# Kernel tuning notes

Measured on AMD Instinct MI355X. Metric: run time of the kernel, lower is better.

Reference implementation:

```python
import jax, jax.numpy as jnp
import numpy as np
from jax import lax

# Dims: B=batch, Cin=in_channel, Ch=channel (bottleneck), Br=breadth (num expert kernels)
B, Cin, Ch, Br, H, W = 16, 256, 128, 8, 64, 64


def setup_inputs() -> dict:
    key = jax.random.key(0)
    ks = jax.random.split(key, 6)
    sc = lambda k, shape: jax.random.normal(k, shape, jnp.float32) * 0.05
    return {
        "x": jax.random.normal(ks[0], (B, Cin, H, W), jnp.float32),
        # SwitchedConv #1: 3x3, in_channel -> channel, breadth expert kernels
        "W1": sc(ks[1], (Br, Ch, Cin, 3, 3)),
        "b1": jnp.zeros((Ch,), jnp.float32),
        # lambda coupler #1: 1x1 projection in_channel -> breadth (per-pixel routing)
        "Wc1": sc(ks[2], (Br, Cin)),
        "bc1": jnp.zeros((Br,), jnp.float32),
        # SwitchedConv #2: 1x1, channel -> in_channel
        "W2": sc(ks[3], (Br, Cin, Ch, 1, 1)),
        "b2": jnp.zeros((Cin,), jnp.float32),
        # lambda coupler #2: 1x1 projection channel -> breadth
        "Wc2": sc(ks[4], (Br, Ch)),
        "bc2": jnp.zeros((Br,), jnp.float32),
    }


def _switched_conv(x, Wk, b, Wc, bc, pad):
    """Input-conditioned mixture of `breadth` conv kernels.

    The coupler (1x1 projection of x to breadth logits, softmax over breadth)
    produces per-pixel mixture weights; each expert kernel's conv output is
    combined per-pixel with these weights.
    x: [B, Cin, H, W]; Wk: [Br, Cout, Cin, k, k]
    """
    br, cout, cin, k, _ = Wk.shape
    bsz, _, h, w = x.shape
    # per-pixel routing weights over the breadth dim: [B, Br, H, W]
    sel = jax.nn.softmax(jnp.einsum('bihw,gi->bghw', x, Wc) + bc[None, :, None, None], axis=1)
    # all breadth branches in one grouped-output conv: [B, Br*Cout, H, W]
    y = lax.conv_general_dilated(
        x, Wk.reshape(br * cout, cin, k, k),
        window_strides=(1, 1), padding=[(pad, pad), (pad, pad)],
        dimension_numbers=('NCHW', 'OIHW', 'NCHW'))
    y = y.reshape(bsz, br, cout, h, w)
    # selection-weighted reduction over breadth + bias
    return jnp.einsum('bgchw,bghw->bchw', y, sel) + b[None, :, None, None]


def reference(x, W1, b1, Wc1, bc1, W2, b2, Wc2, bc2):
    h = jax.nn.relu(x)
    h = _switched_conv(h, W1, b1, Wc1, bc1, pad=1)  # 3x3 switched conv
    h = jax.nn.relu(h)
    h = _switched_conv(h, W2, b2, Wc2, bc2, pad=0)  # 1x1 switched conv
    return h + x  # residual add
```

## Files before the change

kernel.cpp:

```cpp
#include <hip/hip_runtime.h>
#include <hip/hip_bf16.h>
#include <cstdint>

typedef _Float16 h8 __attribute__((ext_vector_type(8)));
typedef _Float16 h4 __attribute__((ext_vector_type(4)));
typedef float    f4 __attribute__((ext_vector_type(4)));
typedef float    fx16 __attribute__((ext_vector_type(16)));


#define GLD16(src, dst) __builtin_amdgcn_global_load_lds( \
    (const __attribute__((address_space(1))) void*)(src), \
    (__attribute__((address_space(3))) void*)(dst), 16, 0, 0)

__global__ __launch_bounds__(256) void prep_w_k(const float* __restrict__ W1,
        const float* __restrict__ W2, _Float16* __restrict__ W1r,
        _Float16* __restrict__ W2r) {
    int o8 = blockIdx.x * 256 + threadIdx.x;
    if (o8 < 294912) {
        int sq = o8 & 3;
        int c  = (o8 >> 2) & 127;
        int g  = (o8 >> 9) & 7;
        int tk = o8 >> 12;
        int tap = tk % 9, cik = tk / 9;
        int s = sq ^ ((c >> 1) & 3);
        int ci0 = cik * 32 + s * 8;
        const float* src = W1 + ((size_t)(g * 128 + c) * 256 + ci0) * 9 + tap;
        h8 v;
        #pragma unroll
        for (int e = 0; e < 8; ++e) v[e] = (_Float16)src[e * 9];
        *(h8*)(W1r + (size_t)o8 * 8) = v;
    } else {
        int ow = o8 - 294912;
        int sg = ow & 3;
        int co = (ow >> 2) & 255;
        int kc = (ow >> 10) & 3;
        int g  = ow >> 12;
        const float* src = W2 + ((size_t)(g * 256 + co) * 128) + kc * 32 + sg * 8;
        h8 v;
        #pragma unroll
        for (int e = 0; e < 8; ++e) v[e] = (_Float16)src[e];
        *(h8*)(W2r + (size_t)ow * 8) = v;
    }
}

__global__ __launch_bounds__(256) void prep_x_k(const float* __restrict__ x,
        const float* __restrict__ Wc1, const float* __restrict__ bc1,
        float* __restrict__ sel1) {
    __shared__ float wc[2048];
    int t = threadIdx.x;
    for (int i = t; i < 2048; i += 256) wc[i] = Wc1[i];
    __syncthreads();
    int pix = blockIdx.x * 256 + t;
    int b = pix >> 12, p = pix & 4095;
    const float* xp = x + (size_t)b * 1048576 + p;
    float lg[8] = {0.f,0.f,0.f,0.f,0.f,0.f,0.f,0.f};
    for (int c = 0; c < 256; ++c) {
        float v = fmaxf(xp[(size_t)c * 4096], 0.f);
        #pragma unroll
        for (int g = 0; g < 8; ++g) lg[g] += wc[g * 256 + c] * v;
    }
    float m = -1e30f;
    #pragma unroll
    for (int g = 0; g < 8; ++g) { lg[g] += bc1[g]; m = fmaxf(m, lg[g]); }
    float sum = 0.f;
    #pragma unroll
    for (int g = 0; g < 8; ++g) { lg[g] = __expf(lg[g] - m); sum += lg[g]; }
    float inv = 1.f / sum;
    #pragma unroll
    for (int g = 0; g < 8; ++g)
        sel1[(size_t)(b * 8 + g) * 4096 + p] = lg[g] * inv;
}

__global__ __launch_bounds__(512, 2) void conv1_k(const float* __restrict__ x,
        const _Float16* __restrict__ W1r, const float* __restrict__ sel1,
        const float* __restrict__ b1, _Float16* __restrict__ hr) {
    __shared__ _Float16 wt[2][32768];
    __shared__ _Float16 xs[12296];
    int t = threadIdx.x;
    int b = blockIdx.y, yt = blockIdx.x;
    int y0 = yt * 4;
    int w = t >> 6, l = t & 63;
    int wm = w >> 2, wn = w & 3;
    int l31 = l & 31, kq2 = l >> 5;
    if (t < 8) xs[12288 + t] = (_Float16)0.f;

    fx16 acc[2][2];
    #pragma unroll
    for (int m = 0; m < 2; ++m)
        #pragma unroll
        for (int n = 0; n < 2; ++n)
            #pragma unroll
            for (int e = 0; e < 16; ++e) acc[m][n][e] = 0.f;

    {
        const _Float16* srcw = W1r + (size_t)t * 8;
        _Float16* dw = wt[0] + t * 8;
        #pragma unroll
        for (int it = 0; it < 8; ++it)
            GLD16(srcw + it * 4096, dw + it * 4096);
    }

    int px[2];
    #pragma unroll
    for (int nf = 0; nf < 2; ++nf) px[nf] = wn * 64 + nf * 32 + l31;
    bool e0 = (l31 == 0), e63 = (l31 == 31);
    int afo[2][2];
    #pragma unroll
    for (int m = 0; m < 2; ++m)
        #pragma unroll
        for (int kc = 0; kc < 2; ++kc) {
            int c = wm * 64 + m * 32 + l31;
            afo[m][kc] = c * 32 + (((kc * 2 + kq2) ^ ((c >> 1) & 3)) * 8);
        }
    int ba[2][3][2];
    #pragma unroll
    for (int nf = 0; nf < 2; ++nf)
        #pragma unroll
        for (int kx = 0; kx < 3; ++kx) {
            int rz = px[nf] + kx - 1;
            #pragma unroll
            for (int kc = 0; kc < 2; ++kc)
                ba[nf][kx][kc] = rz * 32 + (((kc * 2 + kq2) ^ ((rz >> 1) & 3)) * 8);
        }
    h8 selv[2];
    #pragma unroll
    for (int nf = 0; nf < 2; ++nf)
        #pragma unroll
        for (int g = 0; g < 8; ++g)
            selv[nf][g] = (_Float16)sel1[(size_t)(b * 8 + g) * 4096 + yt * 256 + px[nf]];

    #pragma unroll 1
    for (int ci = 0; ci < 8; ++ci) {
        __syncthreads();
        if (t < 384) {
            int r = t >> 6, col = t & 63;
            int rc = r * 64 + col;
            int yi = y0 - 1 + r;
            _Float16* dx = xs + rc * 32;
            int rx = (rc >> 1) & 3;
            if (yi >= 0 && yi < 64) {
                const float* xp = x + ((size_t)(b * 256 + ci * 32)) * 4096 + yi * 64 + col;
                float v[32];
                #pragma unroll
                for (int c2 = 0; c2 < 32; ++c2)
                    v[c2] = fmaxf(xp[(size_t)c2 * 4096], 0.f);
                #pragma unroll
                for (int qq = 0; qq < 4; ++qq) {
                    h8 hv;
                    #pragma unroll
                    for (int e = 0; e < 8; ++e) hv[e] = (_Float16)v[qq * 8 + e];
                    *(h8*)(dx + (qq ^ rx) * 8) = hv;
                }
            } else {
                const h8 HZ = {};
                #pragma unroll
                for (int qq = 0; qq < 4; ++qq)
                    *(h8*)(dx + (qq ^ rx) * 8) = HZ;
            }
        }
        #pragma unroll 1
        for (int ky = 0; ky < 3; ++ky) {
            #pragma unroll
            for (int kx = 0; kx < 3; ++kx) {
                int grp = ci * 9 + ky * 3 + kx;
                __syncthreads();
                if (grp < 71) {
                    const _Float16* srcw = W1r + (size_t)(grp + 1) * 32768 + t * 8;
                    _Float16* dw = wt[(grp + 1) & 1] + t * 8;
                    #pragma unroll
                    for (int it = 0; it < 8; ++it)
                        GLD16(srcw + it * 4096, dw + it * 4096);
                }
                h8 bfr[2][2];
                #pragma unroll
                for (int nf = 0; nf < 2; ++nf)
                    #pragma unroll
                    for (int kc = 0; kc < 2; ++kc) {
                        int a = ba[nf][kx][kc] + ky * 2048;
                        if (kx == 0 && nf == 0) a = e0 ? 12288 : a;
                        if (kx == 2 && nf == 1) a = e63 ? 12288 : a;
                        bfr[nf][kc] = *(const h8*)(xs + a);
                    }
                const _Float16* wp = wt[grp & 1];
                #pragma unroll
                for (int g = 0; g < 8; ++g) {
                    h8 a00 = *(const h8*)(wp + g * 4096 + afo[0][0]);
                    h8 a01 = *(const h8*)(wp + g * 4096 + afo[0][1]);
                    h8 a10 = *(const h8*)(wp + g * 4096 + afo[1][0]);
                    h8 a11 = *(const h8*)(wp + g * 4096 + afo[1][1]);
                    #pragma unroll
                    for (int nf = 0; nf < 2; ++nf) {
                        _Float16 sg = selv[nf][g];
                        h8 b0 = bfr[nf][0] * sg;
                        h8 b1v = bfr[nf][1] * sg;
                        acc[0][nf] = __builtin_amdgcn_mfma_f32_32x32x16_f16(
                            a00, b0, acc[0][nf], 0, 0, 0);
                        acc[1][nf] = __builtin_amdgcn_mfma_f32_32x32x16_f16(
                            a10, b0, acc[1][nf], 0, 0, 0);
                        acc[0][nf] = __builtin_amdgcn_mfma_f32_32x32x16_f16(
                            a01, b1v, acc[0][nf], 0, 0, 0);
                        acc[1][nf] = __builtin_amdgcn_mfma_f32_32x32x16_f16(
                            a11, b1v, acc[1][nf], 0, 0, 0);
                    }
                }
            }
        }
    }
    #pragma unroll
    for (int m = 0; m < 2; ++m)
        #pragma unroll
        for (int nf = 0; nf < 2; ++nf) {
            size_t pg = ((size_t)(b * 4096 + yt * 256 + px[nf])) * 128;
            #pragma unroll
            for (int q = 0; q < 4; ++q) {
                int c0 = wm * 64 + m * 32 + q * 8 + kq2 * 4;
                f4 bb = *(const f4*)(b1 + c0);
                h4 hv;
                #pragma unroll
                for (int r = 0; r < 4; ++r)
                    hv[r] = (_Float16)fmaxf(acc[m][nf][q * 4 + r] + bb[r], 0.f);
                *(h4*)(hr + pg + c0) = hv;
            }
        }
}

__global__ __launch_bounds__(256, 2) void conv2_k(const _Float16* __restrict__ hr,
        const _Float16* __restrict__ W2r, const float* __restrict__ Wc2,
        const float* __restrict__ bc2, const float* __restrict__ b2,
        const float* __restrict__ x, float* __restrict__ out) {
    __shared__ _Float16 hs[64 * 128];
    __shared__ _Float16 wt[2][256 * 32];
    __shared__ float wc[1024];
    __shared__ float red[2048];
    __shared__ float selw[512];
    int t = threadIdx.x;
    int bid = blockIdx.x;
    int b = bid >> 6, p0 = (bid & 63) * 64;
    int l = t & 63, w = t >> 6;
    int wm = w >> 1, wn = w & 1;
    int l15 = l & 15, sl = l >> 4;
    int swl = (l15 & 7) << 3;
    const f4 FZ = {0.f, 0.f, 0.f, 0.f};
    f4 acce[8][2], accf[8][2];
    #pragma unroll
    for (int m = 0; m < 8; ++m)
        #pragma unroll
        for (int n = 0; n < 2; ++n) { acce[m][n] = FZ; accf[m][n] = FZ; }
    for (int i = t; i < 1024; i += 256) wc[i] = Wc2[i];
    {
        int px = t >> 2, qq = t & 3;
        const _Float16* src = hr + (size_t)(b * 4096 + p0 + px) * 128 + qq * 32;
        #pragma unroll
        for (int u = 0; u < 4; ++u)
            *(h8*)(hs + ((px * 128 + qq * 32 + u * 8) ^ ((px & 7) << 3)))
                = *(const h8*)(src + u * 8);
    }
    h8 wr[4];
    auto load_w = [&](int T) {
        const _Float16* srcw = W2r + (size_t)T * 8192;
        #pragma unroll
        for (int it = 0; it < 4; ++it)
            wr[it] = *(const h8*)(srcw + (size_t)(it * 256 + t) * 8);
    };
    auto write_w = [&](int bf) {
        #pragma unroll
        for (int it = 0; it < 4; ++it) {
            int cc = it * 256 + t;
            int c = cc >> 2, q = cc & 3;
            *(h8*)(wt[bf] + ((c * 32 + q * 8) ^ ((c & 7) << 3))) = wr[it];
        }
    };
    load_w(0);
    __syncthreads();
    {
        int px = t >> 2, qq = t & 3;
        float lg[8] = {0.f,0.f,0.f,0.f,0.f,0.f,0.f,0.f};
        #pragma unroll
        for (int u = 0; u < 4; ++u) {
            h8 v = *(const h8*)(hs + ((px * 128 + qq * 32 + u * 8) ^ ((px & 7) << 3)));
            #pragma unroll
            for (int e = 0; e < 8; ++e) {
                float f = (float)v[e];
                int c = qq * 32 + u * 8 + e;
                #pragma unroll
                for (int g = 0; g < 8; ++g) lg[g] += wc[g * 128 + c] * f;
            }
        }
        #pragma unroll
        for (int g = 0; g < 8; ++g) red[(px * 8 + g) * 4 + qq] = lg[g];
    }
    __syncthreads();
    if (t < 64) {
        float lg[8]; float m = -1e30f;
        #pragma unroll
        for (int g = 0; g < 8; ++g) {
            lg[g] = red[(t*8+g)*4+0] + red[(t*8+g)*4+1]
                  + red[(t*8+g)*4+2] + red[(t*8+g)*4+3] + bc2[g];
            m = fmaxf(m, lg[g]);
        }
        float sum = 0.f;
        #pragma unroll
        for (int g = 0; g < 8; ++g) { lg[g] = __expf(lg[g] - m); sum += lg[g]; }
        float inv = 1.f / sum;
        #pragma unroll
        for (int g = 0; g < 8; ++g) selw[t * 8 + g] = lg[g] * inv;
    }
    write_w(0);
    __syncthreads();
    float selr[8][2];
    #pragma unroll
    for (int g = 0; g < 8; ++g)
        #pragma unroll
        for (int n = 0; n < 2; ++n)
            selr[g][n] = selw[(wn * 32 + n * 16 + l15) * 8 + g];
    int afo[8];
    #pragma unroll
    for (int m = 0; m < 8; ++m) {
        int c = wm * 128 + m * 16 + l15;
        afo[m] = ((c * 32 + sl * 8) ^ swl);
    }
    int buf = 0;
    #pragma unroll 1
    for (int T = 0; T < 32; ++T) {
        bool hn = (T < 31);
        if (hn) load_w(T + 1);
        __syncthreads();
        int kc = (T & 3) * 32;
        h8 bfv[2];
        #pragma unroll
        for (int n = 0; n < 2; ++n) {
            int px = wn * 32 + n * 16 + l15;
            bfv[n] = *(const h8*)(hs + ((px * 128 + kc + sl * 8) ^ ((px & 7) << 3)));
        }
        #pragma unroll
        for (int m = 0; m < 8; ++m) {
            h8 af = *(const h8*)(wt[buf] + afo[m]);
            #pragma unroll
            for (int n = 0; n < 2; ++n)
                acce[m][n] = __builtin_amdgcn_mfma_f32_16x16x32_f16(
                    af, bfv[n], acce[m][n], 0, 0, 0);
        }
        if ((T & 3) == 3) {
            int g = T >> 2;
            #pragma unroll
            for (int n = 0; n < 2; ++n)
                #pragma unroll
                for (int m = 0; m < 8; ++m) {
                    accf[m][n] += selr[g][n] * acce[m][n];
                    acce[m][n] = FZ;
                }
        }
        if (hn) write_w(buf ^ 1);
        buf ^= 1;
    }
    #pragma unroll
    for (int m = 0; m < 8; ++m) {
        int c0 = wm * 128 + m * 16 + sl * 4;
        f4 bb = *(const f4*)(b2 + c0);
        #pragma unroll
        for (int n = 0; n < 2; ++n) {
            int px = wn * 32 + n * 16 + l15;
            size_t o = (size_t)(b * 256 + c0) * 4096 + p0 + px;
            #pragma unroll
            for (int r = 0; r < 4; ++r)
                out[o + (size_t)r * 4096] = accf[m][n][r] + bb[r] + x[o + (size_t)r * 4096];
        }
    }
}

extern "C" void kernel_launch(void* const* d_in, const int* in_sizes, int n_in,
                              void* d_out, int out_size, void* d_ws, size_t ws_size,
                              hipStream_t stream) {
    const float* x   = (const float*)d_in[0];
    const float* W1  = (const float*)d_in[1];
    const float* b1  = (const float*)d_in[2];
    const float* Wc1 = (const float*)d_in[3];
    const float* bc1 = (const float*)d_in[4];
    const float* W2  = (const float*)d_in[5];
    const float* b2  = (const float*)d_in[6];
    const float* Wc2 = (const float*)d_in[7];
    const float* bc2 = (const float*)d_in[8];
    float* out = (float*)d_out;
    char* ws = (char*)d_ws;
    _Float16* hr  = (_Float16*)(ws);
    _Float16* W1r = (_Float16*)(ws + 16777216);
    _Float16* W2r = (_Float16*)(ws + 21495808);
    float* sel1   = (float*)(ws + 22020096);

    hipLaunchKernelGGL(prep_w_k, dim3(1280), dim3(256), 0, stream, W1, W2, W1r, W2r);
    hipLaunchKernelGGL(prep_x_k, dim3(256), dim3(256), 0, stream, x, Wc1, bc1, sel1);
    hipLaunchKernelGGL(conv1_k, dim3(16, 16), dim3(512), 0, stream, x, W1r, sel1, b1, hr);
    hipLaunchKernelGGL(conv2_k, dim3(1024), dim3(256), 0, stream, hr, W2r, Wc2, bc2, b2, x, out);
}
```

Before: 348.0 us.

## Pipeline conv1 weight staging in finer chunks with register prefetch

Splits each tap's weight tile into four 2-group chunks and rotates them through a three-buffer LDS ring, issuing async global-to-LDS loads two chunks ahead. A-fragments for the next chunk are preloaded into registers (FA/FB ping-pong) while MFMAs run on the current ones. LDS use drops from 64K to 24K halfs. The cost is four barriers per tap instead of one, plus more register pressure from the 16 preloaded fragments.

```diff
diff --git a/kernel.cpp b/kernel.cpp
--- a/kernel.cpp
+++ b/kernel.cpp
@@ -71,10 +71,38 @@
         sel1[(size_t)(b * 8 + g) * 4096 + p] = lg[g] * inv;
 }
 
+#define MFMA_BLOCK(F, GP) do { \
+    _Pragma("unroll") \
+    for (int gl_ = 0; gl_ < 2; ++gl_) { \
+        _Pragma("unroll") \
+        for (int kc_ = 0; kc_ < 2; ++kc_) { \
+            _Pragma("unroll") \
+            for (int nf_ = 0; nf_ < 2; ++nf_) { \
+                h8 bs_ = bfr[nf_][kc_] * selv[nf_][(GP) * 2 + gl_]; \
+                acc[0][nf_] = __builtin_amdgcn_mfma_f32_32x32x16_f16( \
+                    F[gl_ * 4 + kc_ * 2 + 0], bs_, acc[0][nf_], 0, 0, 0); \
+                acc[1][nf_] = __builtin_amdgcn_mfma_f32_32x32x16_f16( \
+                    F[gl_ * 4 + kc_ * 2 + 1], bs_, acc[1][nf_], 0, 0, 0); \
+            } } } \
+} while (0)
+
+#define PRELOAD(BI, F) do { \
+    const _Float16* wp_ = wt[BI]; \
+    _Pragma("unroll") \
+    for (int gl_ = 0; gl_ < 2; ++gl_) { \
+        _Pragma("unroll") \
+        for (int kc_ = 0; kc_ < 2; ++kc_) { \
+            _Pragma("unroll") \
+            for (int m_ = 0; m_ < 2; ++m_) \
+                F[gl_ * 4 + kc_ * 2 + m_] = \
+                    *(const h8*)(wp_ + gl_ * 4096 + afo[m_][kc_]); \
+        } } \
+} while (0)
+
 __global__ __launch_bounds__(512, 2) void conv1_k(const float* __restrict__ x,
         const _Float16* __restrict__ W1r, const float* __restrict__ sel1,
         const float* __restrict__ b1, _Float16* __restrict__ hr) {
-    __shared__ _Float16 wt[2][32768];
+    __shared__ _Float16 wt[3][8192];
     __shared__ _Float16 xs[12296];
     int t = threadIdx.x;
     int b = blockIdx.y, yt = blockIdx.x;
@@ -92,13 +120,12 @@
             #pragma unroll
             for (int e = 0; e < 16; ++e) acc[m][n][e] = 0.f;
 
-    {
-        const _Float16* srcw = W1r + (size_t)t * 8;
-        _Float16* dw = wt[0] + t * 8;
-        #pragma unroll
-        for (int it = 0; it < 8; ++it)
-            GLD16(srcw + it * 4096, dw + it * 4096);
-    }
+    auto stage_w = [&](int P, int bi) {
+        const _Float16* srcw = W1r + (size_t)P * 8192 + t * 8;
+        _Float16* dw = wt[bi] + t * 8;
+        GLD16(srcw, dw);
+        GLD16(srcw + 4096, dw + 4096);
+    };
 
     int px[2];
     #pragma unroll
@@ -129,9 +156,16 @@
         for (int g = 0; g < 8; ++g)
             selv[nf][g] = (_Float16)sel1[(size_t)(b * 8 + g) * 4096 + yt * 256 + px[nf]];
 
+    h8 FA[8], FB[8];
+    h8 bfr[2][2];
+
+    stage_w(0, 0);
+    stage_w(1, 1);
+    __syncthreads();
+    PRELOAD(0, FA);
+
     #pragma unroll 1
     for (int ci = 0; ci < 8; ++ci) {
-        __syncthreads();
         if (t < 384) {
             int r = t >> 6, col = t & 63;
             int rc = r * 64 + col;
@@ -158,20 +192,12 @@
                     *(h8*)(dx + (qq ^ rx) * 8) = HZ;
             }
         }
+        __syncthreads();
         #pragma unroll 1
         for (int ky = 0; ky < 3; ++ky) {
             #pragma unroll
             for (int kx = 0; kx < 3; ++kx) {
-                int grp = ci * 9 + ky * 3 + kx;
-                __syncthreads();
-                if (grp < 71) {
-                    const _Float16* srcw = W1r + (size_t)(grp + 1) * 32768 + t * 8;
-                    _Float16* dw = wt[(grp + 1) & 1] + t * 8;
-                    #pragma unroll
-                    for (int it = 0; it < 8; ++it)
-                        GLD16(srcw + it * 4096, dw + it * 4096);
-                }
-                h8 bfr[2][2];
+                int P0 = (ci * 9 + ky * 3 + kx) * 4;
                 #pragma unroll
                 for (int nf = 0; nf < 2; ++nf)
                     #pragma unroll
@@ -181,27 +207,18 @@
                         if (kx == 2 && nf == 1) a = e63 ? 12288 : a;
                         bfr[nf][kc] = *(const h8*)(xs + a);
                     }
-                const _Float16* wp = wt[grp & 1];
-                #pragma unroll
-                for (int g = 0; g < 8; ++g) {
-                    h8 a00 = *(const h8*)(wp + g * 4096 + afo[0][0]);
-                    h8 a01 = *(const h8*)(wp + g * 4096 + afo[0][1]);
-                    h8 a10 = *(const h8*)(wp + g * 4096 + afo[1][0]);
-                    h8 a11 = *(const h8*)(wp + g * 4096 + afo[1][1]);
-                    #pragma unroll
-                    for (int nf = 0; nf < 2; ++nf) {
-                        _Float16 sg = selv[nf][g];
-                        h8 b0 = bfr[nf][0] * sg;
-                        h8 b1v = bfr[nf][1] * sg;
-                        acc[0][nf] = __builtin_amdgcn_mfma_f32_32x32x16_f16(
-                            a00, b0, acc[0][nf], 0, 0, 0);
-                        acc[1][nf] = __builtin_amdgcn_mfma_f32_32x32x16_f16(
-                            a10, b0, acc[1][nf], 0, 0, 0);
-                        acc[0][nf] = __builtin_amdgcn_mfma_f32_32x32x16_f16(
-                            a01, b1v, acc[0][nf], 0, 0, 0);
-                        acc[1][nf] = __builtin_amdgcn_mfma_f32_32x32x16_f16(
-                            a11, b1v, acc[1][nf], 0, 0, 0);
+                #pragma unroll
+                for (int gp = 0; gp < 4; ++gp) {
+                    int P = P0 + gp;
+                    if (P < 286) stage_w(P + 2, (kx + gp + 2) % 3);
+                    if (gp & 1) {
+                        if (P < 287) PRELOAD((kx + gp + 1) % 3, FA);
+                        MFMA_BLOCK(FB, gp);
+                    } else {
+                        if (P < 287) PRELOAD((kx + gp + 1) % 3, FB);
+                        MFMA_BLOCK(FA, gp);
                     }
+                    __syncthreads();
                 }
             }
         }
```

Measured after the change: 378.3 us. 1.09x slower.

## Pipeline conv1 weight staging as triple-buffered 16KB chunks with vmcnt waits

Applied to the files above, without the earlier changes.

The 64KB double-buffered weight tile per tap is replaced by a triple buffer of 16KB chunks, each covering two expert groups. Each chunk is prefetched two steps ahead, and a raw s_barrier plus a partial vmcnt wait stands in for the full __syncthreads per tap. LDS use drops from about 152KB to about 73KB, which could allow two blocks per CU, and the loads overlap more finely with the MFMA work. In exchange there are four barriers per tap instead of one, and correctness depends on the hand-written waitcnt counts and buffer-index arithmetic.

```diff
diff --git a/kernel.cpp b/kernel.cpp
--- a/kernel.cpp
+++ b/kernel.cpp
@@ -74,7 +74,7 @@
 __global__ __launch_bounds__(512, 2) void conv1_k(const float* __restrict__ x,
         const _Float16* __restrict__ W1r, const float* __restrict__ sel1,
         const float* __restrict__ b1, _Float16* __restrict__ hr) {
-    __shared__ _Float16 wt[2][32768];
+    __shared__ _Float16 wt[3][8192];
     __shared__ _Float16 xs[12296];
     int t = threadIdx.x;
     int b = blockIdx.y, yt = blockIdx.x;
@@ -92,13 +92,12 @@
             #pragma unroll
             for (int e = 0; e < 16; ++e) acc[m][n][e] = 0.f;
 
-    {
-        const _Float16* srcw = W1r + (size_t)t * 8;
-        _Float16* dw = wt[0] + t * 8;
-        #pragma unroll
-        for (int it = 0; it < 8; ++it)
-            GLD16(srcw + it * 4096, dw + it * 4096);
-    }
+    auto stage_w = [&](int P, int bi) {
+        const _Float16* srcw = W1r + (size_t)P * 8192 + t * 8;
+        _Float16* dw = wt[bi] + t * 8;
+        GLD16(srcw, dw);
+        GLD16(srcw + 4096, dw + 4096);
+    };
 
     int px[2];
     #pragma unroll
@@ -129,9 +128,13 @@
         for (int g = 0; g < 8; ++g)
             selv[nf][g] = (_Float16)sel1[(size_t)(b * 8 + g) * 4096 + yt * 256 + px[nf]];
 
+    h8 bfr[2][2];
+
+    stage_w(0, 0);
+    stage_w(1, 1);
+
     #pragma unroll 1
     for (int ci = 0; ci < 8; ++ci) {
-        __syncthreads();
         if (t < 384) {
             int r = t >> 6, col = t & 63;
             int rc = r * 64 + col;
@@ -158,20 +161,12 @@
                     *(h8*)(dx + (qq ^ rx) * 8) = HZ;
             }
         }
+        __syncthreads();
         #pragma unroll 1
         for (int ky = 0; ky < 3; ++ky) {
             #pragma unroll
             for (int kx = 0; kx < 3; ++kx) {
-                int grp = ci * 9 + ky * 3 + kx;
-                __syncthreads();
-                if (grp < 71) {
-                    const _Float16* srcw = W1r + (size_t)(grp + 1) * 32768 + t * 8;
-                    _Float16* dw = wt[(grp + 1) & 1] + t * 8;
-                    #pragma unroll
-                    for (int it = 0; it < 8; ++it)
-                        GLD16(srcw + it * 4096, dw + it * 4096);
-                }
-                h8 bfr[2][2];
+                int P0 = (ci * 9 + ky * 3 + kx) * 4;
                 #pragma unroll
                 for (int nf = 0; nf < 2; ++nf)
                     #pragma unroll
@@ -181,27 +176,34 @@
                         if (kx == 2 && nf == 1) a = e63 ? 12288 : a;
                         bfr[nf][kc] = *(const h8*)(xs + a);
                     }
-                const _Float16* wp = wt[grp & 1];
-                #pragma unroll
-                for (int g = 0; g < 8; ++g) {
-                    h8 a00 = *(const h8*)(wp + g * 4096 + afo[0][0]);
-                    h8 a01 = *(const h8*)(wp + g * 4096 + afo[0][1]);
-                    h8 a10 = *(const h8*)(wp + g * 4096 + afo[1][0]);
-                    h8 a11 = *(const h8*)(wp + g * 4096 + afo[1][1]);
+                #pragma unroll
+                for (int gp = 0; gp < 4; ++gp) {
+                    int P = P0 + gp;
+                    __builtin_amdgcn_s_barrier();
+                    if (P >= 286) {
+                        asm volatile("s_waitcnt vmcnt(0)" ::: "memory");
+                    } else {
+                        asm volatile("s_waitcnt vmcnt(2)" ::: "memory");
+                    }
+                    __builtin_amdgcn_sched_barrier(0);
+                    const _Float16* wp = wt[(kx + gp) % 3];
                     #pragma unroll
-                    for (int nf = 0; nf < 2; ++nf) {
-                        _Float16 sg = selv[nf][g];
-                        h8 b0 = bfr[nf][0] * sg;
-                        h8 b1v = bfr[nf][1] * sg;
-                        acc[0][nf] = __builtin_amdgcn_mfma_f32_32x32x16_f16(
-                            a00, b0, acc[0][nf], 0, 0, 0);
-                        acc[1][nf] = __builtin_amdgcn_mfma_f32_32x32x16_f16(
-                            a10, b0, acc[1][nf], 0, 0, 0);
-                        acc[0][nf] = __builtin_amdgcn_mfma_f32_32x32x16_f16(
-                            a01, b1v, acc[0][nf], 0, 0, 0);
-                        acc[1][nf] = __builtin_amdgcn_mfma_f32_32x32x16_f16(
-                            a11, b1v, acc[1][nf], 0, 0, 0);
+                    for (int gl = 0; gl < 2; ++gl) {
+                        #pragma unroll
+                        for (int kc = 0; kc < 2; ++kc) {
+                            h8 a0 = *(const h8*)(wp + gl * 4096 + afo[0][kc]);
+                            h8 a1 = *(const h8*)(wp + gl * 4096 + afo[1][kc]);
+                            #pragma unroll
+                            for (int nf = 0; nf < 2; ++nf) {
+                                h8 bs = bfr[nf][kc] * selv[nf][gp * 2 + gl];
+                                acc[0][nf] = __builtin_amdgcn_mfma_f32_32x32x16_f16(
+                                    a0, bs, acc[0][nf], 0, 0, 0);
+                                acc[1][nf] = __builtin_amdgcn_mfma_f32_32x32x16_f16(
+                                    a1, bs, acc[1][nf], 0, 0, 0);
+                            }
+                        }
                     }
+                    if (P < 286) stage_w(P + 2, (kx + gp + 2) % 3);
                 }
             }
         }
```

New measurement: 337.7 us. 3.0% less time.
